# Performance work log

Measured on AMD Instinct MI355X. Metric: run time of the kernel, lower is better.

The kernel has to match this reference:

```python
import jax, jax.numpy as jnp
import numpy as np

B, N, E = 128, 256, 2048
BINS = 16

def _gcn(x, src, dst, W, b):
    # GCNConv with self-loops and symmetric deg^-1/2 normalization (PyG default).
    h = x @ W  # [N, Fout]
    deg = jnp.zeros(x.shape[0], x.dtype).at[dst].add(1.0) + 1.0  # +1 self-loop
    dinv = jax.lax.rsqrt(deg)
    coef = dinv[src] * dinv[dst]  # [E]
    agg = jnp.zeros_like(h).at[dst].add(h[src] * coef[:, None])
    return agg + h / deg[:, None] + b  # self-loop norm = 1/deg

def _gnn(x, ei, W1, b1, W2, b2, W3, b3):
    # x: [B,N,Fin], ei: [B,2,E]. Dropout skipped (eval mode).
    def single(x, ei):
        s, d = ei[0], ei[1]
        h = jax.nn.relu(_gcn(x, s, d, W1, b1))
        h = jax.nn.relu(_gcn(h, s, d, W2, b2))
        return _gcn(h, s, d, W3, b3)
    return jax.vmap(single)(x, ei)

def _att_pool(x, Watt):
    # SimGNN attention pooling; all graphs have exactly N nodes.
    ctx = jnp.tanh((x @ Watt.T).sum(axis=1) / jnp.asarray(N, x.dtype))  # [B,f3]
    scores = jax.nn.sigmoid(jnp.einsum('bnf,bf->bn', x, ctx))  # [B,N]
    return jnp.einsum('bnf,bn->bf', x, scores)  # [B,f3]

def _forward(xq, xc, eq, ec, W1, b1, W2, b2, W3, b3, Watt, ntnW, ntnV, ntnb, fc1W, fc1b, fc2W, fc2b):
    q = _gnn(xq, eq, W1, b1, W2, b2, W3, b3)  # [B,N,f3]
    c = _gnn(xc, ec, W1, b1, W2, b2, W3, b3)
    e1 = _att_pool(q, Watt)
    e2 = _att_pool(c, Watt)
    # NTN: bilinear + linear on concat + bias
    scores = jax.nn.relu(
        jnp.einsum('bi,tij,bj->bt', e1, ntnW, e2)
        + jnp.concatenate([e1, e2], axis=-1) @ ntnV.T
        + ntnb
    )  # [B, tensor_neurons]
    # histogram of all pairwise node-embedding dot products (torch.histc semantics)
    s = jnp.einsum('bnf,bmf->bnm', q, c).ravel()
    lo, hi = s.min(), s.max()
    idx = jnp.clip(jnp.floor((s - lo) / (hi - lo) * BINS).astype(jnp.int32), 0, BINS - 1)
    counts = jnp.zeros(BINS, s.dtype).at[idx].add(1.0)
    h = jax.lax.stop_gradient(counts / counts.sum())
    scores = jnp.concatenate([scores, jnp.broadcast_to(h, (scores.shape[0], BINS))], axis=1)
    scores = jax.nn.relu(scores @ fc1W.T + fc1b)
    p = jax.nn.sigmoid(scores @ fc2W.T + fc2b)  # [B,1]
    return p.squeeze()


def setup_inputs() -> dict:
    key = jax.random.key(0)
    ks = jax.random.split(key, 20)
    Fin, f1, f2, f3, T, BN = 128, 128, 64, 32, 16, 16
    def xav(k, shape):
        fan_in, fan_out = shape[-1], shape[0]
        lim = np.sqrt(6.0 / (fan_in + fan_out))
        return jax.random.uniform(k, shape, jnp.float32, -lim, lim)
    return {
        'xq': jax.random.normal(ks[0], (B, N, Fin), jnp.float32),
        'xc': jax.random.normal(ks[1], (B, N, Fin), jnp.float32),
        'eq': jax.random.randint(ks[2], (B, 2, E), 0, N, jnp.int32),
        'ec': jax.random.randint(ks[3], (B, 2, E), 0, N, jnp.int32),
        'W1': xav(ks[4], (Fin, f1)), 'b1': jnp.zeros((f1,), jnp.float32),
        'W2': xav(ks[5], (f1, f2)), 'b2': jnp.zeros((f2,), jnp.float32),
        'W3': xav(ks[6], (f2, f3)), 'b3': jnp.zeros((f3,), jnp.float32),
        'Watt': xav(ks[7], (f3, f3)),
        'ntnW': xav(ks[8], (T, f3, f3)),
        'ntnV': xav(ks[9], (T, 2 * f3)),
        'ntnb': xav(ks[10], (T, 1)).squeeze(-1),
        'fc1W': xav(ks[11], (BN, T + BINS)), 'fc1b': jnp.zeros((BN,), jnp.float32),
        'fc2W': xav(ks[12], (1, BN)), 'fc2b': jnp.zeros((1,), jnp.float32),
    }


def reference(xq, xc, eq, ec, W1, b1, W2, b2, W3, b3, Watt, ntnW, ntnV, ntnb, fc1W, fc1b, fc2W, fc2b):
    return _forward(xq, xc, eq, ec, W1, b1, W2, b2, W3, b3, Watt, ntnW, ntnV, ntnb, fc1W, fc1b, fc2W, fc2b)
```

## Files before the change

kernel.cpp:

```cpp
#include <hip/hip_runtime.h>
#include <math.h>

#define BB 128
#define NN 256
#define EE 2048
#define BINS 16

__device__ __forceinline__ unsigned int fenc(float f) {
    unsigned int u = __float_as_uint(f);
    return (u & 0x80000000u) ? ~u : (u | 0x80000000u);
}
__device__ __forceinline__ float fdec(unsigned int u) {
    return (u & 0x80000000u) ? __uint_as_float(u & 0x7FFFFFFFu)
                             : __uint_as_float(~u);
}

__global__ void csr_kernel(const int* __restrict__ eq, const int* __restrict__ ec,
                           int* __restrict__ off, int* __restrict__ srcs,
                           float* __restrict__ wts,
                           unsigned int* __restrict__ lohiE,
                           float* __restrict__ counts) {
    int g = blockIdx.x;
    int b = g < BB ? g : g - BB;
    const int* ei = g < BB ? eq : ec;
    int t = threadIdx.x;
    if (g == 0) {
        if (t < BINS) counts[t] = 0.f;
        if (t == 16) lohiE[0] = 0xFFFFFFFFu;
        if (t == 17) lohiE[1] = 0u;
    }
    __shared__ int cnt[NN];
    __shared__ int sa[NN], sb[NN];
    __shared__ int cursor[NN];
    __shared__ float dvs[NN];
    cnt[t] = 0;
    __syncthreads();
    const int* src = ei + b * 2 * EE;
    const int* dst = src + EE;
    for (int e = t; e < EE; e += 256) atomicAdd(&cnt[dst[e]], 1);
    __syncthreads();
    dvs[t] = rsqrtf((float)cnt[t] + 1.0f);
    sa[t] = cnt[t];
    __syncthreads();
    int* pin = sa; int* pout = sb;
    for (int d = 1; d < NN; d <<= 1) {
        int v = pin[t];
        if (t >= d) v += pin[t - d];
        pout[t] = v;
        __syncthreads();
        int* tmp = pin; pin = pout; pout = tmp;
    }
    int excl = pin[t] - cnt[t];
    off[g * 257 + t] = excl;
    if (t == 255) off[g * 257 + 256] = EE;
    cursor[t] = excl;
    __syncthreads();
    for (int e = t; e < EE; e += 256) {
        int d = dst[e], s = src[e];
        int pos = atomicAdd(&cursor[d], 1);
        srcs[g * EE + pos] = s;
        wts[g * EE + pos] = dvs[s] * dvs[d];
    }
}

template<int FIN, int FOUT, bool RELU, int NSPLIT>
__global__ __launch_bounds__(512) void gcn_fused8(
        const float* __restrict__ X0, const float* __restrict__ X1,
        const float* __restrict__ W, const float* __restrict__ bias,
        const int* __restrict__ off, const int* __restrict__ srcs,
        const float* __restrict__ wts, float* __restrict__ OUT) {
    constexpr int CHUNKS = FOUT / 32;
    int blk = blockIdx.x;
    int g = blk % (2 * BB);
    int rest = blk / (2 * BB);
    int cb = (rest % CHUNKS) * 32;
    int half = rest / CHUNKS;
    int t = threadIdx.x;

    __shared__ float hT[NN * 33];
    __shared__ float xsT[16 * 260];
    __shared__ float wt[16 * 32];
    __shared__ int   eoff[NN + 1];
    __shared__ int   esrc[EE];
    __shared__ float ewt[EE];

    const float* xg = (g < BB) ? (X0 + (size_t)g * NN * FIN)
                               : (X1 + (size_t)(g - BB) * NN * FIN);
    const int* o = off + g * 257;
    const int* sr = srcs + (size_t)g * EE;
    const float* wg = wts + (size_t)g * EE;

    for (int i = t; i < EE; i += 512) { esrc[i] = sr[i]; ewt[i] = wg[i]; }
    for (int i = t; i <= NN; i += 512) eoff[i] = o[i];

    int l = t & 63;
    int wv = t >> 6;

    float acc[4][4];
#pragma unroll
    for (int i = 0; i < 4; i++)
#pragma unroll
        for (int j = 0; j < 4; j++) acc[i][j] = 0.f;

    int sn = t >> 1, qk = (t & 1) * 8;
    const float* xr = xg + sn * FIN + qk;
    float4 v0 = *(const float4*)xr;
    float4 v1 = *(const float4*)(xr + 4);
    float wreg = W[(t >> 5) * FOUT + cb + (t & 31)];

    for (int k0 = 0; k0 < FIN; k0 += 16) {
        xsT[(qk + 0) * 260 + sn] = v0.x;
        xsT[(qk + 1) * 260 + sn] = v0.y;
        xsT[(qk + 2) * 260 + sn] = v0.z;
        xsT[(qk + 3) * 260 + sn] = v0.w;
        xsT[(qk + 4) * 260 + sn] = v1.x;
        xsT[(qk + 5) * 260 + sn] = v1.y;
        xsT[(qk + 6) * 260 + sn] = v1.z;
        xsT[(qk + 7) * 260 + sn] = v1.w;
        wt[t] = wreg;
        __syncthreads();
        if (k0 + 16 < FIN) {
            xr += 16;
            v0 = *(const float4*)xr;
            v1 = *(const float4*)(xr + 4);
            wreg = W[(k0 + 16 + (t >> 5)) * FOUT + cb + (t & 31)];
        }
#pragma unroll
        for (int k = 0; k < 16; k++) {
            float4 xv = *(const float4*)&xsT[k * 260 + 4 * l];
            float4 wvv = *(const float4*)&wt[k * 32 + 4 * wv];
            acc[0][0] += xv.x * wvv.x; acc[0][1] += xv.x * wvv.y;
            acc[0][2] += xv.x * wvv.z; acc[0][3] += xv.x * wvv.w;
            acc[1][0] += xv.y * wvv.x; acc[1][1] += xv.y * wvv.y;
            acc[1][2] += xv.y * wvv.z; acc[1][3] += xv.y * wvv.w;
            acc[2][0] += xv.z * wvv.x; acc[2][1] += xv.z * wvv.y;
            acc[2][2] += xv.z * wvv.z; acc[2][3] += xv.z * wvv.w;
            acc[3][0] += xv.w * wvv.x; acc[3][1] += xv.w * wvv.y;
            acc[3][2] += xv.w * wvv.z; acc[3][3] += xv.w * wvv.w;
        }
        __syncthreads();
    }
#pragma unroll
    for (int i = 0; i < 4; i++)
#pragma unroll
        for (int j = 0; j < 4; j++)
            hT[(4 * l + i) * 33 + 4 * wv + j] = acc[i][j];
    __syncthreads();

    int c = t & 31, ng = t >> 5;
    float bb_ = bias[cb + c];
    float* outp = OUT + (size_t)g * NN * FOUT;
    constexpr int NSEG = NN / NSPLIT;
    int nlo = half * NSEG, nhi = nlo + NSEG;
    for (int n = nlo + ng; n < nhi; n += 16) {
        int j0 = eoff[n], j1 = eoff[n + 1];
        float a = 0.f;
        int j = j0;
        if (j < j1) {
            int s0 = esrc[j];
            float w0 = ewt[j];
            for (++j; j < j1; ++j) {
                int s1 = esrc[j];
                float w1 = ewt[j];
                a += hT[s0 * 33 + c] * w0;
                s0 = s1; w0 = w1;
            }
            a += hT[s0 * 33 + c] * w0;
        }
        float d0 = rsqrtf((float)(j1 - j0) + 1.0f);
        float val = a + hT[n * 33 + c] * d0 * d0 + bb_;
        if (RELU) val = fmaxf(val, 0.f);
        outp[n * FOUT + cb + c] = val;
    }
}

__global__ __launch_bounds__(512) void gcn3_att(
        const float* __restrict__ X0, const float* __restrict__ X1,
        const float* __restrict__ W, const float* __restrict__ bias,
        const float* __restrict__ Watt,
        const int* __restrict__ off, const int* __restrict__ srcs,
        const float* __restrict__ wts,
        float* __restrict__ O3, float* __restrict__ e12) {
    constexpr int FIN = 64, FOUT = 32;
    int g = blockIdx.x;
    int t = threadIdx.x;

    __shared__ float hT[NN * 33];
    __shared__ float xsT[16 * 260];
    __shared__ float wt[16 * 32];
    __shared__ int   eoff[NN + 1];
    __shared__ int   esrc[EE];
    __shared__ float ewt[EE];
    float* red    = xsT;
    float* sc     = xsT + 512;
    float* mean_s = xsT + 768;
    float* ctx_s  = xsT + 800;

    const float* xg = (g < BB) ? (X0 + (size_t)g * NN * FIN)
                               : (X1 + (size_t)(g - BB) * NN * FIN);
    const int* o = off + g * 257;
    const int* sr = srcs + (size_t)g * EE;
    const float* wg = wts + (size_t)g * EE;

    for (int i = t; i < EE; i += 512) { esrc[i] = sr[i]; ewt[i] = wg[i]; }
    for (int i = t; i <= NN; i += 512) eoff[i] = o[i];

    int l = t & 63;
    int wv = t >> 6;

    float acc[4][4];
#pragma unroll
    for (int i = 0; i < 4; i++)
#pragma unroll
        for (int j = 0; j < 4; j++) acc[i][j] = 0.f;

    int sn = t >> 1, qk = (t & 1) * 8;
    const float* xr = xg + sn * FIN + qk;
    float4 v0 = *(const float4*)xr;
    float4 v1 = *(const float4*)(xr + 4);
    float wreg = W[(t >> 5) * FOUT + (t & 31)];

    for (int k0 = 0; k0 < FIN; k0 += 16) {
        xsT[(qk + 0) * 260 + sn] = v0.x;
        xsT[(qk + 1) * 260 + sn] = v0.y;
        xsT[(qk + 2) * 260 + sn] = v0.z;
        xsT[(qk + 3) * 260 + sn] = v0.w;
        xsT[(qk + 4) * 260 + sn] = v1.x;
        xsT[(qk + 5) * 260 + sn] = v1.y;
        xsT[(qk + 6) * 260 + sn] = v1.z;
        xsT[(qk + 7) * 260 + sn] = v1.w;
        wt[t] = wreg;
        __syncthreads();
        if (k0 + 16 < FIN) {
            xr += 16;
            v0 = *(const float4*)xr;
            v1 = *(const float4*)(xr + 4);
            wreg = W[(k0 + 16 + (t >> 5)) * FOUT + (t & 31)];
        }
#pragma unroll
        for (int k = 0; k < 16; k++) {
            float4 xv = *(const float4*)&xsT[k * 260 + 4 * l];
            float4 wvv = *(const float4*)&wt[k * 32 + 4 * wv];
            acc[0][0] += xv.x * wvv.x; acc[0][1] += xv.x * wvv.y;
            acc[0][2] += xv.x * wvv.z; acc[0][3] += xv.x * wvv.w;
            acc[1][0] += xv.y * wvv.x; acc[1][1] += xv.y * wvv.y;
            acc[1][2] += xv.y * wvv.z; acc[1][3] += xv.y * wvv.w;
            acc[2][0] += xv.z * wvv.x; acc[2][1] += xv.z * wvv.y;
            acc[2][2] += xv.z * wvv.z; acc[2][3] += xv.z * wvv.w;
            acc[3][0] += xv.w * wvv.x; acc[3][1] += xv.w * wvv.y;
            acc[3][2] += xv.w * wvv.z; acc[3][3] += xv.w * wvv.w;
        }
        __syncthreads();
    }
#pragma unroll
    for (int i = 0; i < 4; i++)
#pragma unroll
        for (int j = 0; j < 4; j++)
            hT[(4 * l + i) * 33 + 4 * wv + j] = acc[i][j];
    __syncthreads();

    int c = t & 31, ng = t >> 5;
    float bb_ = bias[c];
    float A[16];
#pragma unroll
    for (int i = 0; i < 16; i++) {
        int n = ng * 16 + i;
        int j0 = eoff[n], j1 = eoff[n + 1];
        float a = 0.f;
        int j = j0;
        if (j < j1) {
            int s0 = esrc[j];
            float w0 = ewt[j];
            for (++j; j < j1; ++j) {
                int s1 = esrc[j];
                float w1 = ewt[j];
                a += hT[s0 * 33 + c] * w0;
                s0 = s1; w0 = w1;
            }
            a += hT[s0 * 33 + c] * w0;
        }
        float d0 = rsqrtf((float)(j1 - j0) + 1.0f);
        A[i] = a + hT[n * 33 + c] * d0 * d0 + bb_;
    }

    {
        float ps = 0.f;
#pragma unroll
        for (int i = 0; i < 16; i++) ps += A[i];
        red[t] = ps;
    }
    __syncthreads();
    if (t < 32) {
        float m = 0.f;
        for (int p = 0; p < 16; p++) m += red[p * 32 + t];
        mean_s[t] = m / (float)NN;
    }
    __syncthreads();
    if (t < 32) {
        float a = 0.f;
        for (int f = 0; f < 32; f++) a += mean_s[f] * Watt[t * 32 + f];
        ctx_s[t] = tanhf(a);
    }
    __syncthreads();
    {
        float cv = ctx_s[c];
#pragma unroll
        for (int i = 0; i < 16; i++) {
            float v = A[i] * cv;
            v += __shfl_xor(v, 16);
            v += __shfl_xor(v, 8);
            v += __shfl_xor(v, 4);
            v += __shfl_xor(v, 2);
            v += __shfl_xor(v, 1);
            if (c == 0) sc[ng * 16 + i] = 1.f / (1.f + expf(-v));
        }
    }
    __syncthreads();
    {
        float pp = 0.f;
        float* outp = O3 + (size_t)g * NN * 32;
#pragma unroll
        for (int i = 0; i < 16; i++) {
            int n = ng * 16 + i;
            pp += A[i] * sc[n];
            outp[n * 32 + c] = A[i];
        }
        red[t] = pp;
    }
    __syncthreads();
    if (t < 32) {
        float s = 0.f;
        for (int p = 0; p < 16; p++) s += red[p * 32 + t];
        e12[g * 32 + t] = s;
    }
}

#define PD_STAGE_AND_DOT \
    int blk = blockIdx.x; \
    int b = blk >> 2; \
    int tq = (blk >> 1) & 1, tc = blk & 1; \
    __shared__ float qsT[32 * 132]; \
    __shared__ float csT[32 * 132]; \
    int t = threadIdx.x; \
    { \
        int n = t >> 1, f0 = (t & 1) * 16; \
        const float* qp = Q + ((size_t)b * NN + tq * 128 + n) * 32 + f0; \
        const float* cp = C + ((size_t)b * NN + tc * 128 + n) * 32 + f0; \
        float qa16[16], ca16[16]; \
        *(float4*)&qa16[0]  = *(const float4*)(qp); \
        *(float4*)&qa16[4]  = *(const float4*)(qp + 4); \
        *(float4*)&qa16[8]  = *(const float4*)(qp + 8); \
        *(float4*)&qa16[12] = *(const float4*)(qp + 12); \
        *(float4*)&ca16[0]  = *(const float4*)(cp); \
        *(float4*)&ca16[4]  = *(const float4*)(cp + 4); \
        *(float4*)&ca16[8]  = *(const float4*)(cp + 8); \
        *(float4*)&ca16[12] = *(const float4*)(cp + 12); \
        _Pragma("unroll") \
        for (int m = 0; m < 16; m++) { \
            qsT[(f0 + m) * 132 + n] = qa16[m]; \
            csT[(f0 + m) * 132 + n] = ca16[m]; \
        } \
    } \
    __syncthreads(); \
    int rg = (t >> 4) * 4, cg = (t & 15) * 4; \
    float acc[8][8]; \
    _Pragma("unroll") \
    for (int i = 0; i < 8; i++) \
        _Pragma("unroll") \
        for (int j = 0; j < 8; j++) acc[i][j] = 0.f; \
    _Pragma("unroll 2") \
    for (int f = 0; f < 32; f++) { \
        float4 qa = *(const float4*)&qsT[f * 132 + rg]; \
        float4 qb = *(const float4*)&qsT[f * 132 + 64 + rg]; \
        float4 ca = *(const float4*)&csT[f * 132 + cg]; \
        float4 cb = *(const float4*)&csT[f * 132 + 64 + cg]; \
        float qv[8] = {qa.x, qa.y, qa.z, qa.w, qb.x, qb.y, qb.z, qb.w}; \
        float cv[8] = {ca.x, ca.y, ca.z, ca.w, cb.x, cb.y, cb.z, cb.w}; \
        _Pragma("unroll") \
        for (int i = 0; i < 8; i++) \
            _Pragma("unroll") \
            for (int j = 0; j < 8; j++) acc[i][j] += qv[i] * cv[j]; \
    }

__global__ __launch_bounds__(256, 4) void pairdot_minmax(
        const float* __restrict__ Q, const float* __restrict__ C,
        unsigned int* __restrict__ lohiE) {
    PD_STAGE_AND_DOT
    float lmin = acc[0][0], lmax = acc[0][0];
#pragma unroll
    for (int i = 0; i < 8; i++)
#pragma unroll
        for (int j = 0; j < 8; j++) {
            lmin = fminf(lmin, acc[i][j]);
            lmax = fmaxf(lmax, acc[i][j]);
        }
    __shared__ float rmin[256], rmax[256];
    rmin[t] = lmin; rmax[t] = lmax;
    __syncthreads();
    for (int s = 128; s > 0; s >>= 1) {
        if (t < s) { rmin[t] = fminf(rmin[t], rmin[t + s]); rmax[t] = fmaxf(rmax[t], rmax[t + s]); }
        __syncthreads();
    }
    if (t == 0) {
        atomicMin(&lohiE[0], fenc(rmin[0]));
        atomicMax(&lohiE[1], fenc(rmax[0]));
    }
}

__global__ __launch_bounds__(256, 4) void pairdot_hist(
        const float* __restrict__ Q, const float* __restrict__ C,
        const unsigned int* __restrict__ lohiE, float* __restrict__ counts) {
    PD_STAGE_AND_DOT
    float lo = fdec(lohiE[0]), hi = fdec(lohiE[1]);
    float scale = (float)BINS / (hi - lo);
    int lane = t & 63;
    int cnt = 0;
#pragma unroll
    for (int i = 0; i < 8; i++)
#pragma unroll
        for (int j = 0; j < 8; j++) {
            int idx = (int)floorf((acc[i][j] - lo) * scale);
            idx = min(max(idx, 0), BINS - 1);
            unsigned long long b0 = __ballot((idx & 1) != 0);
            unsigned long long b1 = __ballot((idx & 2) != 0);
            unsigned long long b2 = __ballot((idx & 4) != 0);
            unsigned long long b3 = __ballot((idx & 8) != 0);
            unsigned long long msk = ((lane & 1) ? b0 : ~b0);
            msk &= ((lane & 2) ? b1 : ~b1);
            msk &= ((lane & 4) ? b2 : ~b2);
            msk &= ((lane & 8) ? b3 : ~b3);
            cnt += __popcll(msk);
        }
    __shared__ float wbins[4][BINS];
    int wave = t >> 6;
    if (lane < BINS) wbins[wave][lane] = (float)cnt;
    __syncthreads();
    if (t < BINS) {
        atomicAdd(&counts[t], wbins[0][t] + wbins[1][t] + wbins[2][t] + wbins[3][t]);
    }
}

__global__ void final_kernel(const float* __restrict__ e1, const float* __restrict__ e2,
                             const float* __restrict__ ntnW, const float* __restrict__ ntnV,
                             const float* __restrict__ ntnb, const float* __restrict__ counts,
                             const float* __restrict__ fc1W, const float* __restrict__ fc1b,
                             const float* __restrict__ fc2W, const float* __restrict__ fc2b,
                             float* __restrict__ out) {
    int b = blockIdx.x;
    int t = threadIdx.x;
    __shared__ float a1[32], a2[32], red[256], z[32], u[16];
    if (t < 32) a1[t] = e1[b * 32 + t];
    else if (t < 64) a2[t - 32] = e2[b * 32 + t - 32];
    __syncthreads();
    int tt = t >> 4, g = t & 15;
    float p = 0.f;
#pragma unroll
    for (int ii = 0; ii < 2; ii++) {
        int i = g + 16 * ii;
        float d = 0.f;
        const float* wr = ntnW + (tt * 32 + i) * 32;
        for (int j = 0; j < 32; j++) d += wr[j] * a2[j];
        p += a1[i] * d;
    }
    red[t] = p;
    __syncthreads();
    if (t < 16) {
        float s = 0.f;
        for (int g2 = 0; g2 < 16; g2++) s += red[t * 16 + g2];
        float lin = ntnb[t];
        for (int i = 0; i < 32; i++) lin += ntnV[t * 64 + i] * a1[i];
        for (int i = 0; i < 32; i++) lin += ntnV[t * 64 + 32 + i] * a2[i];
        z[t] = fmaxf(s + lin, 0.f);
    } else if (t < 32) {
        float tot = 0.f;
        for (int i = 0; i < BINS; i++) tot += counts[i];
        z[t] = counts[t - 16] / tot;
    }
    __syncthreads();
    if (t < 16) {
        float a = fc1b[t];
        for (int i = 0; i < 32; i++) a += fc1W[t * 32 + i] * z[i];
        u[t] = fmaxf(a, 0.f);
    }
    __syncthreads();
    if (t == 0) {
        float a = fc2b[0];
        for (int i = 0; i < 16; i++) a += fc2W[i] * u[i];
        out[b] = 1.f / (1.f + expf(-a));
    }
}

extern "C" void kernel_launch(void* const* d_in, const int* in_sizes, int n_in,
                              void* d_out, int out_size, void* d_ws, size_t ws_size,
                              hipStream_t stream) {
    const float* xq   = (const float*)d_in[0];
    const float* xc   = (const float*)d_in[1];
    const int*   eq   = (const int*)d_in[2];
    const int*   ec   = (const int*)d_in[3];
    const float* W1   = (const float*)d_in[4];
    const float* b1   = (const float*)d_in[5];
    const float* W2   = (const float*)d_in[6];
    const float* b2   = (const float*)d_in[7];
    const float* W3   = (const float*)d_in[8];
    const float* b3   = (const float*)d_in[9];
    const float* Watt = (const float*)d_in[10];
    const float* ntnW = (const float*)d_in[11];
    const float* ntnV = (const float*)d_in[12];
    const float* ntnb = (const float*)d_in[13];
    const float* fc1W = (const float*)d_in[14];
    const float* fc1b = (const float*)d_in[15];
    const float* fc2W = (const float*)d_in[16];
    const float* fc2b = (const float*)d_in[17];
    float* out = (float*)d_out;
    float* ws  = (float*)d_ws;

    float* O3   = ws;
    float* e12  = O3 + 2097152;
    float* bmin = e12 + 8192;
    float* bmax = bmin + 2048;
    unsigned int* lohiE = (unsigned int*)(bmax + 2048);
    float* cntw = (float*)(lohiE + 2);
    int*   off  = (int*)(ws + 2109504);
    int*   srcs = off + 65792;
    float* wts  = (float*)(srcs + 524288);
    float* O1   = ws + 3223872;
    float* O2   = O1 + 8388608;

    float* O3Q = O3;
    float* O3C = O3 + (size_t)BB * NN * 32;
    float* e1w = e12;
    float* e2w = e12 + BB * 32;
    (void)bmin; (void)bmax;

    csr_kernel<<<2 * BB, 256, 0, stream>>>(eq, ec, off, srcs, wts, lohiE, cntw);

    gcn_fused8<128, 128, true, 1><<<4 * 2 * BB, 512, 0, stream>>>(
        xq, xc, W1, b1, off, srcs, wts, O1);
    gcn_fused8<128, 64, true, 1><<<2 * 2 * BB, 512, 0, stream>>>(
        O1, O1 + (size_t)BB * NN * 128, W2, b2, off, srcs, wts, O2);

    gcn3_att<<<2 * BB, 512, 0, stream>>>(
        O2, O2 + (size_t)BB * NN * 64, W3, b3, Watt, off, srcs, wts, O3, e12);

    pairdot_minmax<<<BB * 4, 256, 0, stream>>>(O3Q, O3C, lohiE);
    pairdot_hist<<<BB * 4, 256, 0, stream>>>(O3Q, O3C, lohiE, cntw);

    final_kernel<<<BB, 256, 0, stream>>>(e1w, e2w, ntnW, ntnV, ntnb, cntw,
                                         fc1W, fc1b, fc2W, fc2b, out);
}
```

Baseline: 280.5 us.

## Fuse pairdot min/max and histogram kernels with a grid-wide spin barrier

```diff
diff --git a/kernel.cpp b/kernel.cpp
--- a/kernel.cpp
+++ b/kernel.cpp
@@ -5,6 +5,7 @@
 #define NN 256
 #define EE 2048
 #define BINS 16
+#define GRID_PD (BB * 4)
 
 __device__ __forceinline__ unsigned int fenc(float f) {
     unsigned int u = __float_as_uint(f);
@@ -19,6 +20,7 @@
                            int* __restrict__ off, int* __restrict__ srcs,
                            float* __restrict__ wts,
                            unsigned int* __restrict__ lohiE,
+                           unsigned int* __restrict__ ticket,
                            float* __restrict__ counts) {
     int g = blockIdx.x;
     int b = g < BB ? g : g - BB;
@@ -28,6 +30,7 @@
         if (t < BINS) counts[t] = 0.f;
         if (t == 16) lohiE[0] = 0xFFFFFFFFu;
         if (t == 17) lohiE[1] = 0u;
+        if (t == 18) ticket[0] = 0u;
     }
     __shared__ int cnt[NN];
     __shared__ int sa[NN], sb[NN];
@@ -335,57 +338,56 @@
     }
 }
 
-#define PD_STAGE_AND_DOT \
-    int blk = blockIdx.x; \
-    int b = blk >> 2; \
-    int tq = (blk >> 1) & 1, tc = blk & 1; \
-    __shared__ float qsT[32 * 132]; \
-    __shared__ float csT[32 * 132]; \
-    int t = threadIdx.x; \
-    { \
-        int n = t >> 1, f0 = (t & 1) * 16; \
-        const float* qp = Q + ((size_t)b * NN + tq * 128 + n) * 32 + f0; \
-        const float* cp = C + ((size_t)b * NN + tc * 128 + n) * 32 + f0; \
-        float qa16[16], ca16[16]; \
-        *(float4*)&qa16[0]  = *(const float4*)(qp); \
-        *(float4*)&qa16[4]  = *(const float4*)(qp + 4); \
-        *(float4*)&qa16[8]  = *(const float4*)(qp + 8); \
-        *(float4*)&qa16[12] = *(const float4*)(qp + 12); \
-        *(float4*)&ca16[0]  = *(const float4*)(cp); \
-        *(float4*)&ca16[4]  = *(const float4*)(cp + 4); \
-        *(float4*)&ca16[8]  = *(const float4*)(cp + 8); \
-        *(float4*)&ca16[12] = *(const float4*)(cp + 12); \
-        _Pragma("unroll") \
-        for (int m = 0; m < 16; m++) { \
-            qsT[(f0 + m) * 132 + n] = qa16[m]; \
-            csT[(f0 + m) * 132 + n] = ca16[m]; \
-        } \
-    } \
-    __syncthreads(); \
-    int rg = (t >> 4) * 4, cg = (t & 15) * 4; \
-    float acc[8][8]; \
-    _Pragma("unroll") \
-    for (int i = 0; i < 8; i++) \
-        _Pragma("unroll") \
-        for (int j = 0; j < 8; j++) acc[i][j] = 0.f; \
-    _Pragma("unroll 2") \
-    for (int f = 0; f < 32; f++) { \
-        float4 qa = *(const float4*)&qsT[f * 132 + rg]; \
-        float4 qb = *(const float4*)&qsT[f * 132 + 64 + rg]; \
-        float4 ca = *(const float4*)&csT[f * 132 + cg]; \
-        float4 cb = *(const float4*)&csT[f * 132 + 64 + cg]; \
-        float qv[8] = {qa.x, qa.y, qa.z, qa.w, qb.x, qb.y, qb.z, qb.w}; \
-        float cv[8] = {ca.x, ca.y, ca.z, ca.w, cb.x, cb.y, cb.z, cb.w}; \
-        _Pragma("unroll") \
-        for (int i = 0; i < 8; i++) \
-            _Pragma("unroll") \
-            for (int j = 0; j < 8; j++) acc[i][j] += qv[i] * cv[j]; \
-    }
-
-__global__ __launch_bounds__(256, 4) void pairdot_minmax(
+__global__ __launch_bounds__(256, 4) void pairdot_all(
         const float* __restrict__ Q, const float* __restrict__ C,
-        unsigned int* __restrict__ lohiE) {
-    PD_STAGE_AND_DOT
+        unsigned int* __restrict__ lohiE, unsigned int* __restrict__ ticket,
+        float* __restrict__ counts) {
+    int blk = blockIdx.x;
+    int b = blk >> 2;
+    int tq = (blk >> 1) & 1, tc = blk & 1;
+    __shared__ float qsT[32 * 132];
+    __shared__ float csT[32 * 132];
+    int t = threadIdx.x;
+    {
+        int n = t >> 1, f0 = (t & 1) * 16;
+        const float* qp = Q + ((size_t)b * NN + tq * 128 + n) * 32 + f0;
+        const float* cp = C + ((size_t)b * NN + tc * 128 + n) * 32 + f0;
+        float qa16[16], ca16[16];
+        *(float4*)&qa16[0]  = *(const float4*)(qp);
+        *(float4*)&qa16[4]  = *(const float4*)(qp + 4);
+        *(float4*)&qa16[8]  = *(const float4*)(qp + 8);
+        *(float4*)&qa16[12] = *(const float4*)(qp + 12);
+        *(float4*)&ca16[0]  = *(const float4*)(cp);
+        *(float4*)&ca16[4]  = *(const float4*)(cp + 4);
+        *(float4*)&ca16[8]  = *(const float4*)(cp + 8);
+        *(float4*)&ca16[12] = *(const float4*)(cp + 12);
+#pragma unroll
+        for (int m = 0; m < 16; m++) {
+            qsT[(f0 + m) * 132 + n] = qa16[m];
+            csT[(f0 + m) * 132 + n] = ca16[m];
+        }
+    }
+    __syncthreads();
+    int rg = (t >> 4) * 4, cg = (t & 15) * 4;
+    float acc[8][8];
+#pragma unroll
+    for (int i = 0; i < 8; i++)
+#pragma unroll
+        for (int j = 0; j < 8; j++) acc[i][j] = 0.f;
+#pragma unroll 2
+    for (int f = 0; f < 32; f++) {
+        float4 qa = *(const float4*)&qsT[f * 132 + rg];
+        float4 qb = *(const float4*)&qsT[f * 132 + 64 + rg];
+        float4 ca = *(const float4*)&csT[f * 132 + cg];
+        float4 cb = *(const float4*)&csT[f * 132 + 64 + cg];
+        float qv[8] = {qa.x, qa.y, qa.z, qa.w, qb.x, qb.y, qb.z, qb.w};
+        float cv[8] = {ca.x, ca.y, ca.z, ca.w, cb.x, cb.y, cb.z, cb.w};
+#pragma unroll
+        for (int i = 0; i < 8; i++)
+#pragma unroll
+            for (int j = 0; j < 8; j++) acc[i][j] += qv[i] * cv[j];
+    }
+
     float lmin = acc[0][0], lmax = acc[0][0];
 #pragma unroll
     for (int i = 0; i < 8; i++)
@@ -395,6 +397,7 @@
             lmax = fmaxf(lmax, acc[i][j]);
         }
     __shared__ float rmin[256], rmax[256];
+    __shared__ float lohi_s[2];
     rmin[t] = lmin; rmax[t] = lmax;
     __syncthreads();
     for (int s = 128; s > 0; s >>= 1) {
@@ -404,14 +407,18 @@
     if (t == 0) {
         atomicMin(&lohiE[0], fenc(rmin[0]));
         atomicMax(&lohiE[1], fenc(rmax[0]));
-    }
-}
-
-__global__ __launch_bounds__(256, 4) void pairdot_hist(
-        const float* __restrict__ Q, const float* __restrict__ C,
-        const unsigned int* __restrict__ lohiE, float* __restrict__ counts) {
-    PD_STAGE_AND_DOT
-    float lo = fdec(lohiE[0]), hi = fdec(lohiE[1]);
+        __threadfence();
+        atomicAdd(ticket, 1u);
+        while (atomicAdd(ticket, 0u) < (unsigned)GRID_PD) {
+            __builtin_amdgcn_s_sleep(8);
+        }
+        __threadfence();
+        lohi_s[0] = fdec(atomicAdd(&lohiE[0], 0u));
+        lohi_s[1] = fdec(atomicAdd(&lohiE[1], 0u));
+    }
+    __syncthreads();
+
+    float lo = lohi_s[0], hi = lohi_s[1];
     float scale = (float)BINS / (hi - lo);
     int lane = t & 63;
     int cnt = 0;
@@ -516,8 +523,8 @@
 
     float* O3   = ws;
     float* e12  = O3 + 2097152;
-    float* bmin = e12 + 8192;
-    float* bmax = bmin + 2048;
+    unsigned int* ticket = (unsigned int*)(e12 + 8192);
+    float* bmax = e12 + 8192 + 2048;
     unsigned int* lohiE = (unsigned int*)(bmax + 2048);
     float* cntw = (float*)(lohiE + 2);
     int*   off  = (int*)(ws + 2109504);
@@ -530,9 +537,9 @@
     float* O3C = O3 + (size_t)BB * NN * 32;
     float* e1w = e12;
     float* e2w = e12 + BB * 32;
-    (void)bmin; (void)bmax;
-
-    csr_kernel<<<2 * BB, 256, 0, stream>>>(eq, ec, off, srcs, wts, lohiE, cntw);
+    (void)bmax;
+
+    csr_kernel<<<2 * BB, 256, 0, stream>>>(eq, ec, off, srcs, wts, lohiE, ticket, cntw);
 
     gcn_fused8<128, 128, true, 1><<<4 * 2 * BB, 512, 0, stream>>>(
         xq, xc, W1, b1, off, srcs, wts, O1);
@@ -542,8 +549,7 @@
     gcn3_att<<<2 * BB, 512, 0, stream>>>(
         O2, O2 + (size_t)BB * NN * 64, W3, b3, Watt, off, srcs, wts, O3, e12);
 
-    pairdot_minmax<<<BB * 4, 256, 0, stream>>>(O3Q, O3C, lohiE);
-    pairdot_hist<<<BB * 4, 256, 0, stream>>>(O3Q, O3C, lohiE, cntw);
+    pairdot_all<<<GRID_PD, 256, 0, stream>>>(O3Q, O3C, lohiE, ticket, cntw);
 
     final_kernel<<<BB, 256, 0, stream>>>(e1w, e2w, ntnW, ntnV, ntnb, cntw,
                                          fc1W, fc1b, fc2W, fc2b, out);
```

After: 296.1 us. 1.06x slower.
